# Optimization experiments

Hardware: AMD Instinct MI355X
Metric: run time of the kernel (lower is better)

## Reference

```python
import jax, jax.numpy as jnp
import numpy as np


def setup_inputs() -> dict:
    key = jax.random.key(0)
    kx, ky = jax.random.split(key)
    n, m, d = 2048, 2048, 16  # d == n_wires
    x = jax.random.normal(kx, (n, d), dtype=jnp.float32)
    y = jax.random.normal(ky, (m, d), dtype=jnp.float32)
    return {"x": x, "y": y}


def reference(x, y):
    # RY gates on distinct wires commute; RY(-y_k) RY(x_k) = RY(x_k - y_k).
    # State = tensor product over wires of RY(x_k - y_k)|0>, so the |0...0>
    # amplitude is prod_k cos((x_k - y_k)/2). Original code stores abs(amplitude).
    half_diff = 0.5 * (x[:, None, :] - y[None, :, :])  # [n, m, d]
    kernel = jnp.abs(jnp.prod(jnp.cos(half_diff), axis=-1))  # [n, m]
    return kernel
```

## Files before the change

kernel.cpp:

```cpp
#include <hip/hip_runtime.h>
#include <hip/hip_bf16.h>


constexpr int D  = 16;
constexpr int BR = 128;
constexpr int BC = 64;
constexpr int BRP = BR + 4;
constexpr int BCP = BC + 4;
constexpr int NT = 256;

__global__ __launch_bounds__(NT)
void qkern(const float* __restrict__ x,
           const float* __restrict__ y,
           float* __restrict__ out,
           int n, int m) {
    __shared__ float cx[D][BRP];
    __shared__ float sx[D][BRP];
    __shared__ float cy[D][BCP];
    __shared__ float sy[D][BCP];

    const int row0 = blockIdx.x * BR;
    const int col0 = blockIdx.y * BC;
    const int tid  = threadIdx.x;

    for (int i = tid; i < BR * D; i += NT) {
        float v = x[(size_t)row0 * D + i];
        int r = i >> 4, k = i & 15;
        float s, c;
        __sincosf(0.5f * v, &s, &c);
        cx[k][r] = c;
        sx[k][r] = s;
    }
    for (int i = tid; i < BC * D; i += NT) {
        float v = y[(size_t)col0 * D + i];
        int r = i >> 4, k = i & 15;
        float s, c;
        __sincosf(0.5f * v, &s, &c);
        cy[k][r] = c;
        sy[k][r] = s;
    }
    __syncthreads();

    const int rg = tid >> 4;
    const int cg = tid & 15;
    const int r0 = rg * 4;
    const int c0 = cg * 4;

    float p[2][4][4];
#pragma unroll
    for (int h = 0; h < 2; ++h)
#pragma unroll
        for (int a = 0; a < 4; ++a)
#pragma unroll
            for (int b = 0; b < 4; ++b)
                p[h][a][b] = 1.0f;

#pragma unroll
    for (int k = 0; k < D; ++k) {
        float4 cxa = *(const float4*)&cx[k][r0];
        float4 sxa = *(const float4*)&sx[k][r0];
        float4 cxb = *(const float4*)&cx[k][r0 + 64];
        float4 sxb = *(const float4*)&sx[k][r0 + 64];
        float4 cyv = *(const float4*)&cy[k][c0];
        float4 syv = *(const float4*)&sy[k][c0];

        const float cxr[8] = {cxa.x, cxa.y, cxa.z, cxa.w,
                              cxb.x, cxb.y, cxb.z, cxb.w};
        const float sxr[8] = {sxa.x, sxa.y, sxa.z, sxa.w,
                              sxb.x, sxb.y, sxb.z, sxb.w};
        const float cyr[4] = {cyv.x, cyv.y, cyv.z, cyv.w};
        const float syr[4] = {syv.x, syv.y, syv.z, syv.w};

#pragma unroll
        for (int a = 0; a < 8; ++a)
#pragma unroll
            for (int b = 0; b < 4; ++b) {
                float t = fmaf(sxr[a], syr[b], cxr[a] * cyr[b]);
                p[a >> 2][a & 3][b] *= t;
            }
    }

#pragma unroll
    for (int h = 0; h < 2; ++h)
#pragma unroll
        for (int a = 0; a < 4; ++a) {
            int row = row0 + r0 + h * 64 + a;
            float4 v;
            v.x = fabsf(p[h][a][0]);
            v.y = fabsf(p[h][a][1]);
            v.z = fabsf(p[h][a][2]);
            v.w = fabsf(p[h][a][3]);
            *(float4*)&out[(size_t)row * m + col0 + c0] = v;
        }
}

extern "C" void kernel_launch(void* const* d_in, const int* in_sizes, int n_in,
                              void* d_out, int out_size, void* d_ws, size_t ws_size,
                              hipStream_t stream) {
    const float* x = (const float*)d_in[0];
    const float* y = (const float*)d_in[1];
    float* out = (float*)d_out;
    const int n = in_sizes[0] / D;
    const int m = in_sizes[1] / D;
    dim3 grid(n / BR, m / BC);
    qkern<<<grid, NT, 0, stream>>>(x, y, out, n, m);
}
```

Measured before the change: 68.92 us.

## Precompute sincos tables in a separate kernel and use register-resident column tiles

Adds a preprocessing kernel that computes cos/sin pairs for x and y once into workspace, with y transposed to k-major layout. The main kernel becomes single-wavefront blocks that keep 16 column cos/sin float4s in registers and read row values with uniform (scalar) loads, dropping shared memory and barriers. Outputs are written with nontemporal stores. This adds a second launch and workspace traffic, and each thread now produces only two outputs per row, so register reuse is lower than the old 8x4 tile.

```diff
diff --git a/kernel.cpp b/kernel.cpp
--- a/kernel.cpp
+++ b/kernel.cpp
@@ -3,95 +3,61 @@
 
 
 constexpr int D  = 16;
-constexpr int BR = 128;
-constexpr int BC = 64;
-constexpr int BRP = BR + 4;
-constexpr int BCP = BC + 4;
-constexpr int NT = 256;
+constexpr int RPB = 16;
+constexpr int CPW = 128;
 
-__global__ __launch_bounds__(NT)
-void qkern(const float* __restrict__ x,
-           const float* __restrict__ y,
-           float* __restrict__ out,
-           int n, int m) {
-    __shared__ float cx[D][BRP];
-    __shared__ float sx[D][BRP];
-    __shared__ float cy[D][BCP];
-    __shared__ float sy[D][BCP];
+typedef float vf2 __attribute__((ext_vector_type(2)));
 
-    const int row0 = blockIdx.x * BR;
-    const int col0 = blockIdx.y * BC;
-    const int tid  = threadIdx.x;
+__global__ __launch_bounds__(256)
+void precs(const float* __restrict__ x, const float* __restrict__ y,
+           float2* __restrict__ csx, float2* __restrict__ csy_t,
+           int nx, int m) {
+    const int gid = blockIdx.x * 256 + threadIdx.x;
+    if (gid < nx) {
+        float s, c;
+        __sincosf(0.5f * x[gid], &s, &c);
+        csx[gid] = make_float2(c, s);
+    } else {
+        const int j = gid - nx;
+        const int k = j / m, col = j - k * m;
+        float s, c;
+        __sincosf(0.5f * y[(size_t)col * D + k], &s, &c);
+        csy_t[j] = make_float2(c, s);
+    }
+}
 
-    for (int i = tid; i < BR * D; i += NT) {
-        float v = x[(size_t)row0 * D + i];
-        int r = i >> 4, k = i & 15;
-        float s, c;
-        __sincosf(0.5f * v, &s, &c);
-        cx[k][r] = c;
-        sx[k][r] = s;
+__global__ __launch_bounds__(64)
+void qkern(const float2* __restrict__ csx, const float2* __restrict__ csy_t,
+           float* __restrict__ out, int m) {
+    const int lane = threadIdx.x;
+    const int col0 = blockIdx.x * CPW + lane * 2;
+    const int rbase = blockIdx.y * RPB;
+
+    float4 colf[D];
+#pragma unroll
+    for (int k = 0; k < D; ++k)
+        colf[k] = *(const float4*)(csy_t + (size_t)k * m + col0);
+
+    const float2* rp = csx + (size_t)rbase * D;
+
+#pragma unroll 4
+    for (int i = 0; i < RPB; ++i) {
+        float p0 = 1.0f, p1 = 1.0f;
+#pragma unroll
+        for (int k = 0; k < D; ++k) {
+            const float cxk = rp[i * D + k].x;
+            const float sxk = rp[i * D + k].y;
+            const float t0 = cxk * colf[k].x + sxk * colf[k].y;
+            const float t1 = cxk * colf[k].z + sxk * colf[k].w;
+            p0 *= t0;
+            p1 *= t1;
+        }
+        vf2 v;
+        v.x = fabsf(p0);
+        v.y = fabsf(p1);
+        __builtin_nontemporal_store(
+            v, (vf2*)(out + (size_t)(rbase + i) * m + col0));
     }
-    for (int i = tid; i < BC * D; i += NT) {
-        float v = y[(size_t)col0 * D + i];
-        int r = i >> 4, k = i & 15;
-        float s, c;
-        __sincosf(0.5f * v, &s, &c);
-        cy[k][r] = c;
-        sy[k][r] = s;
-    }
-    __syncthreads();
-
-    const int rg = tid >> 4;
-    const int cg = tid & 15;
-    const int r0 = rg * 4;
-    const int c0 = cg * 4;
-
-    float p[2][4][4];
-#pragma unroll
-    for (int h = 0; h < 2; ++h)
-#pragma unroll
-        for (int a = 0; a < 4; ++a)
-#pragma unroll
-            for (int b = 0; b < 4; ++b)
-                p[h][a][b] = 1.0f;
-
-#pragma unroll
-    for (int k = 0; k < D; ++k) {
-        float4 cxa = *(const float4*)&cx[k][r0];
-        float4 sxa = *(const float4*)&sx[k][r0];
-        float4 cxb = *(const float4*)&cx[k][r0 + 64];
-        float4 sxb = *(const float4*)&sx[k][r0 + 64];
-        float4 cyv = *(const float4*)&cy[k][c0];
-        float4 syv = *(const float4*)&sy[k][c0];
-
-        const float cxr[8] = {cxa.x, cxa.y, cxa.z, cxa.w,
-                              cxb.x, cxb.y, cxb.z, cxb.w};
-        const float sxr[8] = {sxa.x, sxa.y, sxa.z, sxa.w,
-                              sxb.x, sxb.y, sxb.z, sxb.w};
-        const float cyr[4] = {cyv.x, cyv.y, cyv.z, cyv.w};
-        const float syr[4] = {syv.x, syv.y, syv.z, syv.w};
-
-#pragma unroll
-        for (int a = 0; a < 8; ++a)
-#pragma unroll
-            for (int b = 0; b < 4; ++b) {
-                float t = fmaf(sxr[a], syr[b], cxr[a] * cyr[b]);
-                p[a >> 2][a & 3][b] *= t;
-            }
-    }
-
-#pragma unroll
-    for (int h = 0; h < 2; ++h)
-#pragma unroll
-        for (int a = 0; a < 4; ++a) {
-            int row = row0 + r0 + h * 64 + a;
-            float4 v;
-            v.x = fabsf(p[h][a][0]);
-            v.y = fabsf(p[h][a][1]);
-            v.z = fabsf(p[h][a][2]);
-            v.w = fabsf(p[h][a][3]);
-            *(float4*)&out[(size_t)row * m + col0 + c0] = v;
-        }
 }
 
 extern "C" void kernel_launch(void* const* d_in, const int* in_sizes, int n_in,
@@ -102,6 +68,13 @@
     float* out = (float*)d_out;
     const int n = in_sizes[0] / D;
     const int m = in_sizes[1] / D;
-    dim3 grid(n / BR, m / BC);
-    qkern<<<grid, NT, 0, stream>>>(x, y, out, n, m);
+
+    float2* csx   = (float2*)d_ws;
+    float2* csy_t = (float2*)d_ws + (size_t)n * D;
+
+    const int nx = n * D, ny = m * D;
+    precs<<<(nx + ny + 255) / 256, 256, 0, stream>>>(x, y, csx, csy_t, nx, m);
+
+    dim3 grid(m / CPW, n / RPB);
+    qkern<<<grid, 64, 0, stream>>>(csx, csy_t, out, m);
 }
```

Measured after the change: 73.93 us. +7.3%, slower.
